# Performance work log

Hardware: AMD Instinct MI355X
Metric: run time of the kernel (lower is better)

## Reference

```python
import jax, jax.numpy as jnp
import numpy as np


def setup_inputs() -> dict:
    key = jax.random.key(0)
    k1, k2 = jax.random.split(key)
    B, C, H, W, S = 8, 128, 256, 256, 1024
    inp = jax.random.normal(k1, (B, C, H, W), dtype=jnp.float32)
    seg = jax.random.randint(k2, (B, H, W), 0, S, dtype=jnp.int32)
    return {"input": inp, "segLabels": seg, "num_segments": S}


def reference(input, segLabels, num_segments):
    # input: [B, C, H, W] float; segLabels: [B, H, W] int in [0, S)
    B, C, H, W = input.shape
    S = num_segments
    N = H * W
    # [B, N, C] pixel features
    feats = jnp.transpose(input.reshape(B, C, N), (0, 2, 1))
    # offset labels so each image's segments occupy a disjoint id range
    ids = (segLabels.reshape(B, N) + jnp.arange(B, dtype=segLabels.dtype)[:, None] * S).reshape(-1)
    flat = feats.reshape(B * N, C)
    sums = jax.ops.segment_sum(flat, ids, num_segments=B * S)          # [B*S, C]
    counts = jax.ops.segment_sum(jnp.ones((B * N,), dtype=input.dtype), ids, num_segments=B * S)  # [B*S]
    avg = sums / jnp.maximum(counts, 1.0)[:, None]
    return avg.reshape(B, S, C)
```

## Files before the change

### kernel.cpp

```cpp
#include <hip/hip_runtime.h>


#define BB 8
#define CC 128
#define NPIX 65536
#define SS 1024
#define TILE 4096
#define NTILES (NPIX / TILE)
#define THREADS 1024
#define BUFSZ2 (TILE + TILE / 4)

#define POS_ELEMS (BB * NPIX)
#define OFF_ELEMS (BB * NTILES * SS)

__device__ __forceinline__ int swz2(int e) { return e + (e >> 2); }

__global__ __launch_bounds__(THREADS, 1) void sort_kernel(
    const int* __restrict__ seg, unsigned short* __restrict__ pos,
    unsigned short* __restrict__ tileoff) {
  __shared__ unsigned int hist[SS];
  __shared__ unsigned int wsum[16];
  const int b   = blockIdx.x / NTILES;
  const int t   = blockIdx.x % NTILES;
  const int tid = threadIdx.x;

  hist[tid] = 0u;
  __syncthreads();

  const int base = b * NPIX + t * TILE;
  const int4 lab = reinterpret_cast<const int4*>(seg + base)[tid];
  const unsigned int r0 = atomicAdd(&hist[lab.x], 1u);
  const unsigned int r1 = atomicAdd(&hist[lab.y], 1u);
  const unsigned int r2 = atomicAdd(&hist[lab.z], 1u);
  const unsigned int r3 = atomicAdd(&hist[lab.w], 1u);
  __syncthreads();

  const unsigned int cnt = hist[tid];
  unsigned int v = cnt;
  #pragma unroll
  for (int off = 1; off < 64; off <<= 1) {
    const unsigned int u = __shfl_up(v, off);
    if ((tid & 63) >= off) v += u;
  }
  const int w = tid >> 6;
  if ((tid & 63) == 63) wsum[w] = v;
  __syncthreads();
  if (tid < 16) {
    unsigned int x = wsum[tid];
    #pragma unroll
    for (int off = 1; off < 16; off <<= 1) {
      const unsigned int u = __shfl_up(x, off);
      if (tid >= off) x += u;
    }
    wsum[tid] = x;
  }
  __syncthreads();
  const unsigned int woff = (w == 0) ? 0u : wsum[w - 1];
  const unsigned int excl = woff + v - cnt;
  tileoff[(b * NTILES + t) * SS + tid] = (unsigned short)excl;
  hist[tid] = excl;
  __syncthreads();

  ushort4 p4;
  p4.x = (unsigned short)(hist[lab.x] + r0);
  p4.y = (unsigned short)(hist[lab.y] + r1);
  p4.z = (unsigned short)(hist[lab.z] + r2);
  p4.w = (unsigned short)(hist[lab.w] + r3);
  reinterpret_cast<ushort4*>(pos + base)[tid] = p4;
}

__global__ __launch_bounds__(THREADS, 8) void aggr_kernel(
    const float* __restrict__ inp, const unsigned short* __restrict__ pos,
    const unsigned short* __restrict__ tileoff, float* __restrict__ out) {
  __shared__ float2 buf[BUFSZ2];
  __shared__ unsigned short offl[SS + 2];

  const int b   = blockIdx.x >> 6;
  const int c0  = (blockIdx.x & 63) << 1;
  const int tid = threadIdx.x;
  const int tphase = (blockIdx.x & 1) << 3;

  const float4* __restrict__ pl0 =
      reinterpret_cast<const float4*>(inp + ((size_t)b * CC + c0) * NPIX);
  const ushort4* __restrict__ pos4 =
      reinterpret_cast<const ushort4*>(pos + (size_t)b * NPIX);
  const int Q = NPIX / 4;

  float a0 = 0.f, a1 = 0.f;
  int cnt = 0;

  int t0 = tphase;
  int p0i = t0 * (TILE / 4) + tid;
  float4 cv0 = pl0[p0i], cv1 = pl0[p0i + Q];
  ushort4 cp4 = pos4[p0i];
  unsigned short coff = tileoff[(b * NTILES + t0) * SS + tid];

  for (int k = 0; k < NTILES; ++k) {
    __syncthreads();
    if (tid == 0) offl[SS] = (unsigned short)TILE;
    offl[tid] = coff;
    buf[swz2(cp4.x)] = make_float2(cv0.x, cv1.x);
    buf[swz2(cp4.y)] = make_float2(cv0.y, cv1.y);
    buf[swz2(cp4.z)] = make_float2(cv0.z, cv1.z);
    buf[swz2(cp4.w)] = make_float2(cv0.w, cv1.w);

    const int kn = (k + 1 < NTILES) ? k + 1 : k;
    const int tn = (kn + tphase) & (NTILES - 1);
    const int pn = tn * (TILE / 4) + tid;
    const float4 nv0 = pl0[pn], nv1 = pl0[pn + Q];
    const ushort4 np4 = pos4[pn];
    const unsigned short noff = tileoff[(b * NTILES + tn) * SS + tid];

    __syncthreads();
    const int beg = offl[tid];
    const int end = offl[tid + 1];
    cnt += end - beg;
    int j = beg;
    for (; j + 2 <= end; j += 2) {
      const float2 u = buf[swz2(j)];
      const float2 v = buf[swz2(j + 1)];
      a0 += u.x + v.x; a1 += u.y + v.y;
    }
    if (j < end) {
      const float2 u = buf[swz2(j)];
      a0 += u.x; a1 += u.y;
    }

    cv0 = nv0; cv1 = nv1; cp4 = np4; coff = noff;
  }

  const float inv = 1.0f / (float)max(cnt, 1);
  reinterpret_cast<float2*>(out + ((size_t)(b * SS + tid)) * CC + c0)[0] =
      make_float2(a0 * inv, a1 * inv);
}

__global__ __launch_bounds__(THREADS, 1) void seg_avg_kernel(
    const float* __restrict__ inp, const int* __restrict__ seg,
    float* __restrict__ out) {
  __shared__ float acc[SS * 5];
  const int b   = blockIdx.x >> 5;
  const int c0  = (blockIdx.x & 31) << 2;
  const int tid = threadIdx.x;
  for (int i = tid; i < SS * 5; i += THREADS) acc[i] = 0.0f;
  __syncthreads();
  const float4* __restrict__ p0 =
      reinterpret_cast<const float4*>(inp + ((size_t)b * CC + c0) * NPIX);
  const int4* __restrict__ lab = reinterpret_cast<const int4*>(seg + (size_t)b * NPIX);
  const int Q = NPIX / 4;
  int* iacc = reinterpret_cast<int*>(acc);
  for (int i = 0; i < NPIX / (4 * THREADS); ++i) {
    const int p = i * THREADS + tid;
    const int4 s4 = lab[p];
    const float4 v0 = p0[p], v1 = p0[p + Q], v2 = p0[p + 2 * Q], v3 = p0[p + 3 * Q];
    const int a0 = s4.x * 5, a1 = s4.y * 5, a2 = s4.z * 5, a3 = s4.w * 5;
    unsafeAtomicAdd(&acc[a0 + 0], v0.x); unsafeAtomicAdd(&acc[a0 + 1], v1.x);
    unsafeAtomicAdd(&acc[a0 + 2], v2.x); unsafeAtomicAdd(&acc[a0 + 3], v3.x);
    atomicAdd(&iacc[a0 + 4], 1);
    unsafeAtomicAdd(&acc[a1 + 0], v0.y); unsafeAtomicAdd(&acc[a1 + 1], v1.y);
    unsafeAtomicAdd(&acc[a1 + 2], v2.y); unsafeAtomicAdd(&acc[a1 + 3], v3.y);
    atomicAdd(&iacc[a1 + 4], 1);
    unsafeAtomicAdd(&acc[a2 + 0], v0.z); unsafeAtomicAdd(&acc[a2 + 1], v1.z);
    unsafeAtomicAdd(&acc[a2 + 2], v2.z); unsafeAtomicAdd(&acc[a2 + 3], v3.z);
    atomicAdd(&iacc[a2 + 4], 1);
    unsafeAtomicAdd(&acc[a3 + 0], v0.w); unsafeAtomicAdd(&acc[a3 + 1], v1.w);
    unsafeAtomicAdd(&acc[a3 + 2], v2.w); unsafeAtomicAdd(&acc[a3 + 3], v3.w);
    atomicAdd(&iacc[a3 + 4], 1);
  }
  __syncthreads();
  for (int i = tid; i < SS * 4; i += THREADS) {
    const int s = i >> 2, c = i & 3;
    const float cntf = (float)iacc[s * 5 + 4];
    out[((size_t)(b * SS + s)) * CC + c0 + c] = acc[s * 5 + c] / fmaxf(cntf, 1.0f);
  }
}

extern "C" void kernel_launch(void* const* d_in, const int* in_sizes, int n_in,
                              void* d_out, int out_size, void* d_ws, size_t ws_size,
                              hipStream_t stream) {
  const float* inp = (const float*)d_in[0];
  const int*   seg = (const int*)d_in[1];
  float*       out = (float*)d_out;

  const size_t need = (size_t)POS_ELEMS * 2 + (size_t)OFF_ELEMS * 2;
  if (ws_size >= need) {
    unsigned short* pos  = (unsigned short*)d_ws;
    unsigned short* toff = pos + POS_ELEMS;
    sort_kernel<<<BB * NTILES, THREADS, 0, stream>>>(seg, pos, toff);
    aggr_kernel<<<BB * (CC / 2), THREADS, 0, stream>>>(inp, pos, toff, out);
  } else {
    seg_avg_kernel<<<BB * (CC / 4), THREADS, 0, stream>>>(inp, seg, out);
  }
}
```

Before: 369.6 us.

## Replace LDS scatter-gather with global gather via per-tile sorted pixel order

The sort kernel now emits, for each tile, the pixel indices sorted by segment instead of each pixel's sorted position. The aggregation kernel drops its shared-memory scatter buffer and barriers, and each thread instead gathers its segment's pixels directly from global memory using that order. This removes LDS traffic and synchronisation but replaces coalesced float4 loads with scattered 4-byte global gathers, relying on cache hits within each tile.

```diff
diff --git a/kernel.cpp b/kernel.cpp
--- a/kernel.cpp
+++ b/kernel.cpp
@@ -8,18 +8,16 @@
 #define TILE 4096
 #define NTILES (NPIX / TILE)
 #define THREADS 1024
-#define BUFSZ2 (TILE + TILE / 4)
 
-#define POS_ELEMS (BB * NPIX)
+#define ORD_ELEMS (BB * NPIX)
 #define OFF_ELEMS (BB * NTILES * SS)
 
-__device__ __forceinline__ int swz2(int e) { return e + (e >> 2); }
-
 __global__ __launch_bounds__(THREADS, 1) void sort_kernel(
-    const int* __restrict__ seg, unsigned short* __restrict__ pos,
+    const int* __restrict__ seg, unsigned short* __restrict__ ord,
     unsigned short* __restrict__ tileoff) {
   __shared__ unsigned int hist[SS];
   __shared__ unsigned int wsum[16];
+  __shared__ unsigned short obuf[TILE];
   const int b   = blockIdx.x / NTILES;
   const int t   = blockIdx.x % NTILES;
   const int tid = threadIdx.x;
@@ -61,76 +59,61 @@
   hist[tid] = excl;
   __syncthreads();
 
-  ushort4 p4;
-  p4.x = (unsigned short)(hist[lab.x] + r0);
-  p4.y = (unsigned short)(hist[lab.y] + r1);
-  p4.z = (unsigned short)(hist[lab.z] + r2);
-  p4.w = (unsigned short)(hist[lab.w] + r3);
-  reinterpret_cast<ushort4*>(pos + base)[tid] = p4;
+  const int px = tid << 2;
+  obuf[hist[lab.x] + r0] = (unsigned short)(px + 0);
+  obuf[hist[lab.y] + r1] = (unsigned short)(px + 1);
+  obuf[hist[lab.z] + r2] = (unsigned short)(px + 2);
+  obuf[hist[lab.w] + r3] = (unsigned short)(px + 3);
+  __syncthreads();
+
+  reinterpret_cast<ushort4*>(ord + base)[tid] =
+      reinterpret_cast<const ushort4*>(obuf)[tid];
 }
 
 __global__ __launch_bounds__(THREADS, 8) void aggr_kernel(
-    const float* __restrict__ inp, const unsigned short* __restrict__ pos,
+    const float* __restrict__ inp, const unsigned short* __restrict__ ord,
     const unsigned short* __restrict__ tileoff, float* __restrict__ out) {
-  __shared__ float2 buf[BUFSZ2];
-  __shared__ unsigned short offl[SS + 2];
-
   const int b   = blockIdx.x >> 6;
   const int c0  = (blockIdx.x & 63) << 1;
-  const int tid = threadIdx.x;
-  const int tphase = (blockIdx.x & 1) << 3;
+  const int s   = threadIdx.x;
 
-  const float4* __restrict__ pl0 =
-      reinterpret_cast<const float4*>(inp + ((size_t)b * CC + c0) * NPIX);
-  const ushort4* __restrict__ pos4 =
-      reinterpret_cast<const ushort4*>(pos + (size_t)b * NPIX);
-  const int Q = NPIX / 4;
+  const float* __restrict__ pl0 = inp + ((size_t)b * CC + c0) * NPIX;
+  const float* __restrict__ pl1 = pl0 + NPIX;
+  const unsigned short* __restrict__ obase = ord + b * NPIX;
+  const unsigned short* __restrict__ tob = tileoff + b * NTILES * SS;
 
   float a0 = 0.f, a1 = 0.f;
   int cnt = 0;
 
-  int t0 = tphase;
-  int p0i = t0 * (TILE / 4) + tid;
-  float4 cv0 = pl0[p0i], cv1 = pl0[p0i + Q];
-  ushort4 cp4 = pos4[p0i];
-  unsigned short coff = tileoff[(b * NTILES + t0) * SS + tid];
+  #pragma unroll 2
+  for (int t = 0; t < NTILES; ++t) {
+    const int tb = t * TILE;
+    const unsigned short* __restrict__ to = tob + t * SS;
+    const int beg = to[s];
+    const int end = (s == SS - 1) ? TILE : (int)to[s + 1];
+    cnt += end - beg;
+    const unsigned short* __restrict__ o = obase + tb;
 
-  for (int k = 0; k < NTILES; ++k) {
-    __syncthreads();
-    if (tid == 0) offl[SS] = (unsigned short)TILE;
-    offl[tid] = coff;
-    buf[swz2(cp4.x)] = make_float2(cv0.x, cv1.x);
-    buf[swz2(cp4.y)] = make_float2(cv0.y, cv1.y);
-    buf[swz2(cp4.z)] = make_float2(cv0.z, cv1.z);
-    buf[swz2(cp4.w)] = make_float2(cv0.w, cv1.w);
-
-    const int kn = (k + 1 < NTILES) ? k + 1 : k;
-    const int tn = (kn + tphase) & (NTILES - 1);
-    const int pn = tn * (TILE / 4) + tid;
-    const float4 nv0 = pl0[pn], nv1 = pl0[pn + Q];
-    const ushort4 np4 = pos4[pn];
-    const unsigned short noff = tileoff[(b * NTILES + tn) * SS + tid];
-
-    __syncthreads();
-    const int beg = offl[tid];
-    const int end = offl[tid + 1];
-    cnt += end - beg;
     int j = beg;
     for (; j + 2 <= end; j += 2) {
-      const float2 u = buf[swz2(j)];
-      const float2 v = buf[swz2(j + 1)];
-      a0 += u.x + v.x; a1 += u.y + v.y;
+      const int p0 = o[j];
+      const int p1 = o[j + 1];
+      const float x0 = pl0[tb + p0];
+      const float y0 = pl1[tb + p0];
+      const float x1 = pl0[tb + p1];
+      const float y1 = pl1[tb + p1];
+      a0 += x0 + x1;
+      a1 += y0 + y1;
     }
     if (j < end) {
-      const float2 u = buf[swz2(j)];
-      a0 += u.x; a1 += u.y;
+      const int p = o[j];
+      a0 += pl0[tb + p];
+      a1 += pl1[tb + p];
     }
-
-    cv0 = nv0; cv1 = nv1; cp4 = np4; coff = noff;
   }
 
   const float inv = 1.0f / (float)max(cnt, 1);
-  reinterpret_cast<float2*>(out + ((size_t)(b * SS + tid)) * CC + c0)[0] =
+  reinterpret_cast<float2*>(out + ((size_t)(b * SS + s)) * CC + c0)[0] =
       make_float2(a0 * inv, a1 * inv);
 }
 
@@ -181,12 +164,12 @@
   const int*   seg = (const int*)d_in[1];
   float*       out = (float*)d_out;
 
-  const size_t need = (size_t)POS_ELEMS * 2 + (size_t)OFF_ELEMS * 2;
+  const size_t need = (size_t)ORD_ELEMS * 2 + (size_t)OFF_ELEMS * 2;
   if (ws_size >= need) {
-    unsigned short* pos  = (unsigned short*)d_ws;
-    unsigned short* toff = pos + POS_ELEMS;
-    sort_kernel<<<BB * NTILES, THREADS, 0, stream>>>(seg, pos, toff);
-    aggr_kernel<<<BB * (CC / 2), THREADS, 0, stream>>>(inp, pos, toff, out);
+    unsigned short* ord  = (unsigned short*)d_ws;
+    unsigned short* toff = ord + ORD_ELEMS;
+    sort_kernel<<<BB * NTILES, THREADS, 0, stream>>>(seg, ord, toff);
+    aggr_kernel<<<BB * (CC / 2), THREADS, 0, stream>>>(inp, ord, toff, out);
   } else {
     seg_avg_kernel<<<BB * (CC / 4), THREADS, 0, stream>>>(inp, seg, out);
   }
```

After: 579.3 us. +56.7%, slower.

## Double-buffer LDS tiles with one barrier per iteration and halve tile size

Applied to the files above, without the earlier changes.

The aggregation kernel now keeps two shared-memory tile buffers. It scatters tile k while reducing tile k-1, which cuts the barriers per iteration from two to one, using a raw s_waitcnt/s_barrier. Tiles shrink to 2048 pixels, so the sort kernel and per-tile offsets change to match. The padded index is replaced by an XOR swizzle. The trade is more loop iterations and more offset data against fewer synchronisation stalls.

```diff
diff --git a/kernel.cpp b/kernel.cpp
--- a/kernel.cpp
+++ b/kernel.cpp
@@ -5,15 +5,18 @@
 #define CC 128
 #define NPIX 65536
 #define SS 1024
-#define TILE 4096
+#define TILE 2048
 #define NTILES (NPIX / TILE)
 #define THREADS 1024
-#define BUFSZ2 (TILE + TILE / 4)
 
 #define POS_ELEMS (BB * NPIX)
 #define OFF_ELEMS (BB * NTILES * SS)
 
-__device__ __forceinline__ int swz2(int e) { return e + (e >> 2); }
+__device__ __forceinline__ int swz(int e) { return e ^ ((e >> 3) & 7); }
+
+__device__ __forceinline__ void lds_barrier() {
+  asm volatile("s_waitcnt lgkmcnt(0)\n\ts_barrier" ::: "memory");
+}
 
 __global__ __launch_bounds__(THREADS, 1) void sort_kernel(
     const int* __restrict__ seg, unsigned short* __restrict__ pos,
@@ -28,11 +31,9 @@
   __syncthreads();
 
   const int base = b * NPIX + t * TILE;
-  const int4 lab = reinterpret_cast<const int4*>(seg + base)[tid];
+  const int2 lab = reinterpret_cast<const int2*>(seg + base)[tid];
   const unsigned int r0 = atomicAdd(&hist[lab.x], 1u);
   const unsigned int r1 = atomicAdd(&hist[lab.y], 1u);
-  const unsigned int r2 = atomicAdd(&hist[lab.z], 1u);
-  const unsigned int r3 = atomicAdd(&hist[lab.w], 1u);
   __syncthreads();
 
   const unsigned int cnt = hist[tid];
@@ -61,76 +62,92 @@
   hist[tid] = excl;
   __syncthreads();
 
-  ushort4 p4;
-  p4.x = (unsigned short)(hist[lab.x] + r0);
-  p4.y = (unsigned short)(hist[lab.y] + r1);
-  p4.z = (unsigned short)(hist[lab.z] + r2);
-  p4.w = (unsigned short)(hist[lab.w] + r3);
-  reinterpret_cast<ushort4*>(pos + base)[tid] = p4;
+  ushort2 p2;
+  p2.x = (unsigned short)(hist[lab.x] + r0);
+  p2.y = (unsigned short)(hist[lab.y] + r1);
+  reinterpret_cast<ushort2*>(pos + base)[tid] = p2;
 }
 
 __global__ __launch_bounds__(THREADS, 8) void aggr_kernel(
     const float* __restrict__ inp, const unsigned short* __restrict__ pos,
     const unsigned short* __restrict__ tileoff, float* __restrict__ out) {
-  __shared__ float2 buf[BUFSZ2];
-  __shared__ unsigned short offl[SS + 2];
+  __shared__ float2 buf[2][TILE];
+  __shared__ unsigned short offl[2][SS + 1];
 
   const int b   = blockIdx.x >> 6;
   const int c0  = (blockIdx.x & 63) << 1;
-  const int tid = threadIdx.x;
-  const int tphase = (blockIdx.x & 1) << 3;
-
-  const float4* __restrict__ pl0 =
-      reinterpret_cast<const float4*>(inp + ((size_t)b * CC + c0) * NPIX);
-  const ushort4* __restrict__ pos4 =
-      reinterpret_cast<const ushort4*>(pos + (size_t)b * NPIX);
-  const int Q = NPIX / 4;
+  const int s   = threadIdx.x;
+  const int tphase = (blockIdx.x & 1) ? (NTILES / 2) : 0;
+
+  const float* __restrict__ pl0 = inp + ((size_t)b * CC + c0) * NPIX;
+  const float* __restrict__ pl1 = pl0 + NPIX;
+  const unsigned short* __restrict__ pbase = pos + b * NPIX;
+  const unsigned short* __restrict__ tob = tileoff + b * NTILES * SS;
 
   float a0 = 0.f, a1 = 0.f;
   int cnt = 0;
 
-  int t0 = tphase;
-  int p0i = t0 * (TILE / 4) + tid;
-  float4 cv0 = pl0[p0i], cv1 = pl0[p0i + Q];
-  ushort4 cp4 = pos4[p0i];
-  unsigned short coff = tileoff[(b * NTILES + t0) * SS + tid];
+  int tcur = tphase;
+  float2 cv0 = reinterpret_cast<const float2*>(pl0 + tcur * TILE)[s];
+  float2 cv1 = reinterpret_cast<const float2*>(pl1 + tcur * TILE)[s];
+  ushort2 cp = reinterpret_cast<const ushort2*>(pbase + tcur * TILE)[s];
+  unsigned short coff = tob[tcur * SS + s];
 
   for (int k = 0; k < NTILES; ++k) {
-    __syncthreads();
-    if (tid == 0) offl[SS] = (unsigned short)TILE;
-    offl[tid] = coff;
-    buf[swz2(cp4.x)] = make_float2(cv0.x, cv1.x);
-    buf[swz2(cp4.y)] = make_float2(cv0.y, cv1.y);
-    buf[swz2(cp4.z)] = make_float2(cv0.z, cv1.z);
-    buf[swz2(cp4.w)] = make_float2(cv0.w, cv1.w);
+    const int cur = k & 1;
+    const int prv = cur ^ 1;
+
+    if (s == 0) offl[cur][SS] = (unsigned short)TILE;
+    offl[cur][s] = coff;
+    buf[cur][swz(cp.x)] = make_float2(cv0.x, cv1.x);
+    buf[cur][swz(cp.y)] = make_float2(cv0.y, cv1.y);
 
     const int kn = (k + 1 < NTILES) ? k + 1 : k;
     const int tn = (kn + tphase) & (NTILES - 1);
-    const int pn = tn * (TILE / 4) + tid;
-    const float4 nv0 = pl0[pn], nv1 = pl0[pn + Q];
-    const ushort4 np4 = pos4[pn];
-    const unsigned short noff = tileoff[(b * NTILES + tn) * SS + tid];
-
-    __syncthreads();
-    const int beg = offl[tid];
-    const int end = offl[tid + 1];
+    const float2 nv0 = reinterpret_cast<const float2*>(pl0 + tn * TILE)[s];
+    const float2 nv1 = reinterpret_cast<const float2*>(pl1 + tn * TILE)[s];
+    const ushort2 np = reinterpret_cast<const ushort2*>(pbase + tn * TILE)[s];
+    const unsigned short noff = tob[tn * SS + s];
+
+    if (k > 0) {
+      const int beg = offl[prv][s];
+      const int end = offl[prv][s + 1];
+      cnt += end - beg;
+      int j = beg;
+      for (; j + 2 <= end; j += 2) {
+        const float2 u = buf[prv][swz(j)];
+        const float2 v = buf[prv][swz(j + 1)];
+        a0 += u.x + v.x; a1 += u.y + v.y;
+      }
+      if (j < end) {
+        const float2 u = buf[prv][swz(j)];
+        a0 += u.x; a1 += u.y;
+      }
+    }
+
+    lds_barrier();
+    cv0 = nv0; cv1 = nv1; cp = np; coff = noff;
+  }
+
+  {
+    const int prv = (NTILES - 1) & 1;
+    const int beg = offl[prv][s];
+    const int end = offl[prv][s + 1];
     cnt += end - beg;
     int j = beg;
     for (; j + 2 <= end; j += 2) {
-      const float2 u = buf[swz2(j)];
-      const float2 v = buf[swz2(j + 1)];
+      const float2 u = buf[prv][swz(j)];
+      const float2 v = buf[prv][swz(j + 1)];
       a0 += u.x + v.x; a1 += u.y + v.y;
     }
     if (j < end) {
-      const float2 u = buf[swz2(j)];
+      const float2 u = buf[prv][swz(j)];
       a0 += u.x; a1 += u.y;
     }
-
-    cv0 = nv0; cv1 = nv1; cp4 = np4; coff = noff;
   }
 
   const float inv = 1.0f / (float)max(cnt, 1);
-  reinterpret_cast<float2*>(out + ((size_t)(b * SS + tid)) * CC + c0)[0] =
+  reinterpret_cast<float2*>(out + ((size_t)(b * SS + s)) * CC + c0)[0] =
       make_float2(a0 * inv, a1 * inv);
 }
 
```

Measured after the change: 368.3 us. About the same (-0.4%).
